# Kernel optimization log

Measured on AMD Instinct MI355X. Metric: run time of the kernel, lower is better.

Reference implementation:

```python
import jax, jax.numpy as jnp
import numpy as np

DZ, H, DH = 128, 4, 32
DC = H * DH
B, L, N = 1, 256, 256


def setup_inputs() -> dict:
    key = jax.random.key(0)
    ks = jax.random.split(key, 12)
    s = 0.02
    return {
        "z_inter": jax.random.normal(ks[0], (B, L, N, DZ), jnp.float32),
        "dist": jax.random.uniform(ks[1], (B, L, N, N), jnp.float32) * 16.0,
        "ln_g": jnp.ones((DZ,), jnp.float32),
        "ln_b": jnp.zeros((DZ,), jnp.float32),
        "Wq": jax.random.normal(ks[2], (DZ, DC), jnp.float32) * s,
        "bq": jnp.zeros((DC,), jnp.float32),
        "Wk": jax.random.normal(ks[3], (DZ, DC), jnp.float32) * s,
        "bk": jnp.zeros((DC,), jnp.float32),
        "Wv": jax.random.normal(ks[4], (DZ, DC), jnp.float32) * s,
        "bv": jnp.zeros((DC,), jnp.float32),
        "Wg": jax.random.normal(ks[5], (DZ, DC), jnp.float32) * s,
        "bg": jnp.zeros((DC,), jnp.float32),
        "Wo": jax.random.normal(ks[6], (DC, DZ), jnp.float32) * s,
        "bo": jnp.zeros((DZ,), jnp.float32),
    }


def reference(z_inter, dist, ln_g, ln_b, Wq, bq, Wk, bk, Wv, bv, Wg, bg, Wo, bo):
    # LayerNorm over channel dim (eps matches torch default 1e-5)
    mu = jnp.mean(z_inter, axis=-1, keepdims=True)
    var = jnp.mean(jnp.square(z_inter - mu), axis=-1, keepdims=True)
    z = (z_inter - mu) / jnp.sqrt(var + 1e-5) * ln_g + ln_b  # [B,L,N,DZ]

    shp = z.shape[:-1] + (H, DH)
    q = (z @ Wq + bq).reshape(shp)  # [B,L,N,H,DH]
    k = (z @ Wk + bk).reshape(shp)
    v = (z @ Wv + bv).reshape(shp)

    scalar = 1.0 / jnp.sqrt(jnp.asarray(DH, q.dtype))
    attn = jnp.einsum('blihc,bljhc->blihj', q * scalar, k)  # [B,L,N,H,N]

    # Gaussian distance coefficient applied multiplicatively pre-softmax
    coef = jnp.exp(-jnp.square(dist / 8.0) / 2.0)[:, :, :, None, :].astype(q.dtype)
    attn = attn * coef

    attn_weights = jax.nn.softmax(attn, axis=-1)
    v_avg = jnp.einsum('blihj,bljhc->blihc', attn_weights, v)  # [B,L,N,H,DH]

    gate = jax.nn.sigmoid((z @ Wg + bg).reshape(shp))
    z_com = (v_avg * gate).reshape(z.shape[:-1] + (DC,))  # [B,L,N,DC]
    return z_com @ Wo + bo  # [B,L,N,DZ]
```

## Files before the change

### kernel.cpp

```cpp
#include <hip/hip_runtime.h>
#include <hip/hip_fp16.h>

#define LDIM 256
#define NDIM 256
#define DZC  128
#define HN   4
#define DHD  32
#define DCC  128
#define MROWS (LDIM*NDIM)

typedef _Float16 f16;
typedef _Float16 f16x2 __attribute__((ext_vector_type(2)));
typedef _Float16 f16x4 __attribute__((ext_vector_type(4)));
typedef _Float16 f16x8 __attribute__((ext_vector_type(8)));
typedef __fp16   h16x2 __attribute__((ext_vector_type(2)));
typedef float    f32x4 __attribute__((ext_vector_type(4)));

#define SCAL 0.17677669529663687f
#define CEXP -0.011270992135622957f
#define CPRE 0.2550340490960039f

__device__ inline f16x2 pkrtz(float a, float b){
  h16x2 r = __builtin_amdgcn_cvt_pkrtz(a, b);
  union { h16x2 h; f16x2 f; } u; u.h = r;
  return u.f;
}

__global__ __launch_bounds__(256) void k0b_pack(
    const float* __restrict__ Wq, const float* __restrict__ Wk,
    const float* __restrict__ Wv, const float* __restrict__ Wg,
    const float* __restrict__ Wo, f16* __restrict__ w16)
{
  const float* Ws[5] = {Wq, Wk, Wv, Wg, Wo};
  const int tid = blockIdx.x * 256 + threadIdx.x;
  const int p = tid >> 14, rem = tid & 16383;
  const int e = rem & 7, lane = (rem >> 3) & 63, ksjt = rem >> 9;
  const int ks = ksjt & 3, jt = ksjt >> 2;
  const int col = jt*16 + (lane & 15);
  const int k   = ks*32 + (lane >> 4)*8 + e;
  w16[tid] = (f16)Ws[p][k*128 + col];
}

__global__ __launch_bounds__(256, 2) void k1_ln_qkvg(
    const float* __restrict__ z, const float* __restrict__ lng, const float* __restrict__ lnb,
    const f16* __restrict__ w16,
    const float* __restrict__ bq, const float* __restrict__ bk,
    const float* __restrict__ bv, const float* __restrict__ bg,
    f16* __restrict__ qb, f16* __restrict__ kbuf,
    f16* __restrict__ vbuf, f16* __restrict__ gateb)
{
  __shared__ f16 zl[64*128];
  const int t = threadIdx.x;
  const int w = t >> 6, lane = t & 63;
  const int m = lane & 15, g = lane >> 4;
  const int row0 = blockIdx.x * 64;

  {
    const int r = t >> 2, part = t & 3;
    const float* zr = z + (size_t)(row0 + r)*DZC + part*32;
    float vals[32];
    float s = 0.f, sq = 0.f;
    #pragma unroll
    for (int i = 0; i < 8; ++i) {
      float4 v4 = reinterpret_cast<const float4*>(zr)[i];
      vals[i*4+0]=v4.x; vals[i*4+1]=v4.y; vals[i*4+2]=v4.z; vals[i*4+3]=v4.w;
      s  += v4.x+v4.y+v4.z+v4.w;
      sq += v4.x*v4.x + v4.y*v4.y + v4.z*v4.z + v4.w*v4.w;
    }
    s  += __shfl_xor(s, 1);  sq += __shfl_xor(sq, 1);
    s  += __shfl_xor(s, 2);  sq += __shfl_xor(sq, 2);
    const float mu  = s * (1.f/DZC);
    const float var = sq * (1.f/DZC) - mu*mu;
    const float rstd = rsqrtf(var + 1e-5f);
    const float* gg = lng + part*32;
    const float* bb = lnb + part*32;
    #pragma unroll
    for (int i = 0; i < 4; ++i) {
      f16x8 o;
      #pragma unroll
      for (int e = 0; e < 8; ++e)
        o[e] = (f16)((vals[i*8+e]-mu)*rstd*gg[i*8+e] + bb[i*8+e]);
      *reinterpret_cast<f16x8*>(zl + r*128 + (((part*4+i) ^ (r&7))*8)) = o;
    }
  }
  __syncthreads();

  const f16* wp = w16 + w*16384;
  f32x4 acc[4][8];
  #pragma unroll
  for (int it=0;it<4;++it)
    #pragma unroll
    for (int jt=0;jt<8;++jt) acc[it][jt] = (f32x4){0.f,0.f,0.f,0.f};

  #pragma unroll
  for (int ks = 0; ks < 4; ++ks) {
    f16x8 af[8];
    #pragma unroll
    for (int jt=0;jt<8;++jt)
      af[jt] = *reinterpret_cast<const f16x8*>(wp + ((jt*4+ks)*64 + lane)*8);
    f16x8 bf[4];
    #pragma unroll
    for (int it=0;it<4;++it)
      bf[it] = *reinterpret_cast<const f16x8*>(zl + (it*16+m)*128 + (((ks*4+g) ^ (m&7))*8));
    #pragma unroll
    for (int it=0;it<4;++it)
      #pragma unroll
      for (int jt=0;jt<8;++jt)
        acc[it][jt] = __builtin_amdgcn_mfma_f32_16x16x32_f16(af[jt], bf[it], acc[it][jt], 0,0,0);
  }

  const float* bsp = (w==0) ? bq : (w==1) ? bk : (w==2) ? bv : bg;
  float4 bias[8];
  #pragma unroll
  for (int jt=0;jt<8;++jt)
    bias[jt] = *reinterpret_cast<const float4*>(bsp + jt*16 + g*4);

  f16* ob = (w==0) ? qb : (w==1) ? kbuf : (w==2) ? vbuf : gateb;
  #pragma unroll
  for (int it=0;it<4;++it) {
    f16* orow = ob + (size_t)(row0 + it*16 + m)*DCC;
    #pragma unroll
    for (int jt=0;jt<8;++jt) {
      f16x4 o;
      #pragma unroll
      for (int r=0;r<4;++r) {
        float v = acc[it][jt][r] + ((const float*)&bias[jt])[r];
        if (w == 3) v = 1.f/(1.f + __expf(-v));
        o[r] = (f16)v;
      }
      *reinterpret_cast<f16x4*>(orow + jt*16 + g*4) = o;
    }
  }
}

__global__ __launch_bounds__(256, 2) void k2_attn(
    const f16* __restrict__ qb, const f16* __restrict__ kbuf,
    const f16* __restrict__ vbuf, const f16* __restrict__ gateb,
    const float* __restrict__ dist, const f16* __restrict__ wo16,
    const float* __restrict__ bo, float* __restrict__ out)
{
  __shared__ f16 vt[4*32*256];
  __shared__ float cfl[64*64];
  const int t = threadIdx.x;
  const int w = t >> 6, lane = t & 63;
  const int m = lane & 15, g = lane >> 4;
  const int orig = blockIdx.x;
  const int swz = (orig & 7)*64 + (orig >> 3);
  const int l = swz >> 1, half = swz & 1;
  const int r0 = half*128;
  const int lrow0 = l*NDIM;

  {
    #pragma unroll
    for (int hh = 0; hh < 4; ++hh) {
      const f16* vr = vbuf + (size_t)(lrow0 + t)*DCC + hh*DHD;
      #pragma unroll
      for (int p = 0; p < 4; ++p) {
        f16x8 v = *reinterpret_cast<const f16x8*>(vr + p*8);
        #pragma unroll
        for (int e = 0; e < 8; ++e) {
          const int c = p*8 + e;
          vt[hh*8192 + c*256 + (((t>>2) ^ (c&15))*4) + (t&3)] = v[e];
        }
      }
    }
  }

  f16x8 aq[8];
  #pragma unroll
  for (int it = 0; it < 8; ++it)
    aq[it] = *reinterpret_cast<const f16x8*>(
        qb + (size_t)(lrow0 + r0 + it*16 + m)*DCC + w*DHD + g*8);

  f32x4 o[8][2];
  float rs[8];
  #pragma unroll
  for (int it = 0; it < 8; ++it) {
    o[it][0] = (f32x4){0.f,0.f,0.f,0.f};
    o[it][1] = (f32x4){0.f,0.f,0.f,0.f};
    rs[it] = 0.f;
  }

  const float* drow = dist + (size_t)l*(NDIM*NDIM);
  const int prow[4] = { (0*256+t) >> 4, (1*256+t) >> 4, (2*256+t) >> 4, (3*256+t) >> 4 };
  const int pf4  = t & 15;

  float4 pf[4];
  #pragma unroll
  for (int p = 0; p < 4; ++p)
    pf[p] = *reinterpret_cast<const float4*>(
        drow + (size_t)(r0 + prow[p])*NDIM + pf4*4);

  __syncthreads();

  const f16* vth = vt + w*8192;

  #pragma unroll 1
  for (int jc = 0; jc < 4; ++jc) {
    f16x8 kf[4];
    #pragma unroll
    for (int jt = 0; jt < 4; ++jt)
      kf[jt] = *reinterpret_cast<const f16x8*>(
          kbuf + (size_t)(lrow0 + jc*64 + jt*16 + m)*DCC + w*DHD + g*8);

    f16x8 bvv[2][2];
    #pragma unroll
    for (int kc = 0; kc < 2; ++kc)
      #pragma unroll
      for (int ct = 0; ct < 2; ++ct) {
        const int c = ct*16 + m;
        const f16x4 lo = *reinterpret_cast<const f16x4*>(
            vth + c*256 + (((jc*16 + (2*kc+0)*4 + g) ^ m) * 4));
        const f16x4 hi = *reinterpret_cast<const f16x4*>(
            vth + c*256 + (((jc*16 + (2*kc+1)*4 + g) ^ m) * 4));
        f16x8 bb;
        #pragma unroll
        for (int e = 0; e < 4; ++e) { bb[e] = lo[e]; bb[4+e] = hi[e]; }
        bvv[kc][ct] = bb;
      }

    #pragma unroll
    for (int rh = 0; rh < 2; ++rh) {
      __syncthreads();
      float4 d0 = pf[0], d1 = pf[1], d2 = pf[2], d3 = pf[3];
      {
        const int si1 = jc*2 + rh + 1;
        const int sic = (si1 > 7) ? 7 : si1;
        const int jn = sic >> 1, rn = sic & 1;
        #pragma unroll
        for (int p = 0; p < 4; ++p)
          pf[p] = *reinterpret_cast<const float4*>(
              drow + (size_t)(r0 + rn*64 + prow[p])*NDIM + jn*64 + pf4*4);
      }
      {
        const float4 dd[4] = {d0, d1, d2, d3};
        #pragma unroll
        for (int p = 0; p < 4; ++p) {
          const int row = prow[p];
          float4 cf4;
          cf4.x = CPRE * exp2f(dd[p].x*dd[p].x*CEXP);
          cf4.y = CPRE * exp2f(dd[p].y*dd[p].y*CEXP);
          cf4.z = CPRE * exp2f(dd[p].z*dd[p].z*CEXP);
          cf4.w = CPRE * exp2f(dd[p].w*dd[p].w*CEXP);
          *reinterpret_cast<float4*>(cfl + row*64 + ((pf4 ^ (row & 15))*4)) = cf4;
        }
      }
      __syncthreads();

      #pragma unroll
      for (int itl = 0; itl < 4; ++itl) {
        const int it = rh*4 + itl;
        const int lr = itl*16 + m;
        float4 cl[4];
        #pragma unroll
        for (int jt = 0; jt < 4; ++jt)
          cl[jt] = *reinterpret_cast<const float4*>(
              cfl + lr*64 + (((jt*4 + g) ^ m)*4));

        f32x4 s[4];
        #pragma unroll
        for (int jt = 0; jt < 4; ++jt)
          s[jt] = __builtin_amdgcn_mfma_f32_16x16x32_f16(
              kf[jt], aq[it], (f32x4){0.f,0.f,0.f,0.f}, 0, 0, 0);

        f16x2 pk[4][2];
        #pragma unroll
        for (int jt = 0; jt < 4; ++jt) {
          const float p0 = exp2f(s[jt][0] * cl[jt].x);
          const float p1 = exp2f(s[jt][1] * cl[jt].y);
          const float p2 = exp2f(s[jt][2] * cl[jt].z);
          const float p3 = exp2f(s[jt][3] * cl[jt].w);
          rs[it] += (p0 + p1) + (p2 + p3);
          pk[jt][0] = pkrtz(p0, p1);
          pk[jt][1] = pkrtz(p2, p3);
        }

        #pragma unroll
        for (int kc = 0; kc < 2; ++kc) {
          const f16x4 x = __builtin_shufflevector(pk[2*kc  ][0], pk[2*kc  ][1], 0,1,2,3);
          const f16x4 y = __builtin_shufflevector(pk[2*kc+1][0], pk[2*kc+1][1], 0,1,2,3);
          const f16x8 ap = __builtin_shufflevector(x, y, 0,1,2,3,4,5,6,7);
          o[it][0] = __builtin_amdgcn_mfma_f32_16x16x32_f16(ap, bvv[kc][0], o[it][0], 0, 0, 0);
          o[it][1] = __builtin_amdgcn_mfma_f32_16x16x32_f16(ap, bvv[kc][1], o[it][1], 0, 0, 0);
        }
      }
    }
  }

  float rinv[8];
  #pragma unroll
  for (int it = 0; it < 8; ++it) {
    float v = rs[it];
    v += __shfl_xor(v, 16);
    v += __shfl_xor(v, 32);
    rinv[it] = 1.f / v;
  }

  __syncthreads();
  f16* zc = vt;
  #pragma unroll
  for (int it = 0; it < 8; ++it)
    #pragma unroll
    for (int r = 0; r < 4; ++r) {
      const float rr = __shfl(rinv[it], (lane & 48) + g*4 + r);
      const int lrow = it*16 + g*4 + r;
      #pragma unroll
      for (int ct = 0; ct < 2; ++ct)
        zc[lrow*132 + w*DHD + ct*16 + m] = (f16)(o[it][ct][r] * rr);
    }
  __syncthreads();

  f32x4 acc2[2][8];
  #pragma unroll
  for (int it2=0;it2<2;++it2)
    #pragma unroll
    for (int jt=0;jt<8;++jt) acc2[it2][jt] = (f32x4){0.f,0.f,0.f,0.f};

  #pragma unroll
  for (int ks = 0; ks < 4; ++ks) {
    f16x8 af[8];
    #pragma unroll
    for (int jt=0;jt<8;++jt)
      af[jt] = *reinterpret_cast<const f16x8*>(wo16 + ((jt*4+ks)*64 + lane)*8);
    f16x8 bf[2];
    #pragma unroll
    for (int it2 = 0; it2 < 2; ++it2) {
      const int lrow = w*32 + it2*16 + m;
      const f16x4 b0 = *reinterpret_cast<const f16x4*>(zc + lrow*132 + ks*32 + g*8);
      const f16x4 b1 = *reinterpret_cast<const f16x4*>(zc + lrow*132 + ks*32 + g*8 + 4);
      const f16x8 zf = __builtin_shufflevector(b0, b1, 0,1,2,3,4,5,6,7);
      const f16x8 gf = *reinterpret_cast<const f16x8*>(
          gateb + (size_t)(lrow0 + r0 + lrow)*DCC + ks*32 + g*8);
      bf[it2] = zf * gf;
    }
    #pragma unroll
    for (int it2=0;it2<2;++it2)
      #pragma unroll
      for (int jt=0;jt<8;++jt)
        acc2[it2][jt] = __builtin_amdgcn_mfma_f32_16x16x32_f16(af[jt], bf[it2], acc2[it2][jt], 0,0,0);
  }

  #pragma unroll
  for (int it2 = 0; it2 < 2; ++it2) {
    const size_t grow = (size_t)(lrow0 + r0 + w*32 + it2*16 + m);
    #pragma unroll
    for (int jt = 0; jt < 8; ++jt) {
      const float4 bias = *reinterpret_cast<const float4*>(bo + jt*16 + g*4);
      float4 ov;
      ov.x = acc2[it2][jt][0] + bias.x;
      ov.y = acc2[it2][jt][1] + bias.y;
      ov.z = acc2[it2][jt][2] + bias.z;
      ov.w = acc2[it2][jt][3] + bias.w;
      *reinterpret_cast<float4*>(out + grow*DZC + jt*16 + g*4) = ov;
    }
  }
}

extern "C" void kernel_launch(void* const* d_in, const int* in_sizes, int n_in,
                              void* d_out, int out_size, void* d_ws, size_t ws_size,
                              hipStream_t stream) {
  const float* z    = (const float*)d_in[0];
  const float* dist = (const float*)d_in[1];
  const float* lng  = (const float*)d_in[2];
  const float* lnb  = (const float*)d_in[3];
  const float* Wq   = (const float*)d_in[4];
  const float* bq   = (const float*)d_in[5];
  const float* Wk   = (const float*)d_in[6];
  const float* bk   = (const float*)d_in[7];
  const float* Wv   = (const float*)d_in[8];
  const float* bv   = (const float*)d_in[9];
  const float* Wg   = (const float*)d_in[10];
  const float* bg   = (const float*)d_in[11];
  const float* Wo   = (const float*)d_in[12];
  const float* bo   = (const float*)d_in[13];
  float* out = (float*)d_out;

  const size_t elems = (size_t)MROWS * DCC;
  f16* qb    = (f16*)d_ws;
  f16* kbuf  = qb    + elems;
  f16* vbuf  = kbuf  + elems;
  f16* gateb = vbuf  + elems;
  f16* w16   = gateb + elems;

  k0b_pack<<<320, 256, 0, stream>>>(Wq, Wk, Wv, Wg, Wo, w16);
  k1_ln_qkvg<<<MROWS/64, 256, 0, stream>>>(z, lng, lnb, w16, bq, bk, bv, bg,
                                           qb, kbuf, vbuf, gateb);
  k2_attn<<<LDIM*2, 256, 0, stream>>>(qb, kbuf, vbuf, gateb, dist,
                                      w16 + 4*16384, bo, out);
}
```

Measured before the change: 94.01 us.

## Compute softmax exponent in fp16 and double-buffer fp16 distance coefficients

```diff
diff --git a/kernel.cpp b/kernel.cpp
--- a/kernel.cpp
+++ b/kernel.cpp
@@ -19,6 +19,8 @@
 #define SCAL 0.17677669529663687f
 #define CEXP -0.011270992135622957f
 #define CPRE 0.2550340490960039f
+
+extern "C" __device__ _Float16 __ocml_exp2_f16(_Float16);
 
 __device__ inline f16x2 pkrtz(float a, float b){
   h16x2 r = __builtin_amdgcn_cvt_pkrtz(a, b);
@@ -140,7 +142,7 @@
     const float* __restrict__ bo, float* __restrict__ out)
 {
   __shared__ f16 vt[4*32*256];
-  __shared__ float cfl[64*64];
+  __shared__ f16 cfl[2][64*64];
   const int t = threadIdx.x;
   const int w = t >> 6, lane = t & 63;
   const int m = lane & 15, g = lane >> 4;
@@ -221,8 +223,20 @@
 
     #pragma unroll
     for (int rh = 0; rh < 2; ++rh) {
-      __syncthreads();
-      float4 d0 = pf[0], d1 = pf[1], d2 = pf[2], d3 = pf[3];
+      f16* cflc = &cfl[rh][0];
+      {
+        const float4 dd[4] = {pf[0], pf[1], pf[2], pf[3]};
+        #pragma unroll
+        for (int p = 0; p < 4; ++p) {
+          const int row = prow[p];
+          const f16x2 a = pkrtz(CPRE*exp2f(dd[p].x*dd[p].x*CEXP),
+                                CPRE*exp2f(dd[p].y*dd[p].y*CEXP));
+          const f16x2 b = pkrtz(CPRE*exp2f(dd[p].z*dd[p].z*CEXP),
+                                CPRE*exp2f(dd[p].w*dd[p].w*CEXP));
+          const f16x4 cf = __builtin_shufflevector(a, b, 0,1,2,3);
+          *reinterpret_cast<f16x4*>(cflc + row*64 + ((pf4 ^ (row & 15))*4)) = cf;
+        }
+      }
       {
         const int si1 = jc*2 + rh + 1;
         const int sic = (si1 > 7) ? 7 : si1;
@@ -232,30 +246,17 @@
           pf[p] = *reinterpret_cast<const float4*>(
               drow + (size_t)(r0 + rn*64 + prow[p])*NDIM + jn*64 + pf4*4);
       }
-      {
-        const float4 dd[4] = {d0, d1, d2, d3};
-        #pragma unroll
-        for (int p = 0; p < 4; ++p) {
-          const int row = prow[p];
-          float4 cf4;
-          cf4.x = CPRE * exp2f(dd[p].x*dd[p].x*CEXP);
-          cf4.y = CPRE * exp2f(dd[p].y*dd[p].y*CEXP);
-          cf4.z = CPRE * exp2f(dd[p].z*dd[p].z*CEXP);
-          cf4.w = CPRE * exp2f(dd[p].w*dd[p].w*CEXP);
-          *reinterpret_cast<float4*>(cfl + row*64 + ((pf4 ^ (row & 15))*4)) = cf4;
-        }
-      }
       __syncthreads();
 
       #pragma unroll
       for (int itl = 0; itl < 4; ++itl) {
         const int it = rh*4 + itl;
         const int lr = itl*16 + m;
-        float4 cl[4];
+        f16x4 cl[4];
         #pragma unroll
         for (int jt = 0; jt < 4; ++jt)
-          cl[jt] = *reinterpret_cast<const float4*>(
-              cfl + lr*64 + (((jt*4 + g) ^ m)*4));
+          cl[jt] = *reinterpret_cast<const f16x4*>(
+              cflc + lr*64 + (((jt*4 + g) ^ m)*4));
 
         f32x4 s[4];
         #pragma unroll
@@ -263,23 +264,33 @@
           s[jt] = __builtin_amdgcn_mfma_f32_16x16x32_f16(
               kf[jt], aq[it], (f32x4){0.f,0.f,0.f,0.f}, 0, 0, 0);
 
-        f16x2 pk[4][2];
+        f16x4 pkk[4];
         #pragma unroll
         for (int jt = 0; jt < 4; ++jt) {
-          const float p0 = exp2f(s[jt][0] * cl[jt].x);
-          const float p1 = exp2f(s[jt][1] * cl[jt].y);
-          const float p2 = exp2f(s[jt][2] * cl[jt].z);
-          const float p3 = exp2f(s[jt][3] * cl[jt].w);
-          rs[it] += (p0 + p1) + (p2 + p3);
-          pk[jt][0] = pkrtz(p0, p1);
-          pk[jt][1] = pkrtz(p2, p3);
+          const f16x2 sl = pkrtz(s[jt][0], s[jt][1]);
+          const f16x2 sh = pkrtz(s[jt][2], s[jt][3]);
+          const f16x2 cll = __builtin_shufflevector(cl[jt], cl[jt], 0,1);
+          const f16x2 clh = __builtin_shufflevector(cl[jt], cl[jt], 2,3);
+          const f16x2 xl = sl * cll;
+          const f16x2 xh = sh * clh;
+          f16x4 pv;
+          pv[0] = __ocml_exp2_f16(xl[0]);
+          pv[1] = __ocml_exp2_f16(xl[1]);
+          pv[2] = __ocml_exp2_f16(xh[0]);
+          pv[3] = __ocml_exp2_f16(xh[1]);
+          pkk[jt] = pv;
         }
+        {
+          const f16x4 ps4 = (pkk[0] + pkk[1]) + (pkk[2] + pkk[3]);
+          const f16x2 ps2 = __builtin_shufflevector(ps4, ps4, 0,1)
+                          + __builtin_shufflevector(ps4, ps4, 2,3);
+          rs[it] += (float)ps2[0] + (float)ps2[1];
+        }
 
         #pragma unroll
         for (int kc = 0; kc < 2; ++kc) {
-          const f16x4 x = __builtin_shufflevector(pk[2*kc  ][0], pk[2*kc  ][1], 0,1,2,3);
-          const f16x4 y = __builtin_shufflevector(pk[2*kc+1][0], pk[2*kc+1][1], 0,1,2,3);
-          const f16x8 ap = __builtin_shufflevector(x, y, 0,1,2,3,4,5,6,7);
+          const f16x8 ap = __builtin_shufflevector(pkk[2*kc], pkk[2*kc+1],
+                                                   0,1,2,3,4,5,6,7);
           o[it][0] = __builtin_amdgcn_mfma_f32_16x16x32_f16(ap, bvv[kc][0], o[it][0], 0, 0, 0);
           o[it][1] = __builtin_amdgcn_mfma_f32_16x16x32_f16(ap, bvv[kc][1], o[it][1], 0, 0, 0);
         }
```

New measurement: 86.49 us. 8.0% less time.
